# Kernel tuning notes

Measured on AMD Instinct MI355X. Metric: run time of the kernel, lower is better.

## Reference

```python
import jax, jax.numpy as jnp
import numpy as np

B, S, R, A, DW, DR = 64, 32, 128, 64, 512, 512

def setup_inputs() -> dict:
    key = jax.random.key(0)
    ks = jax.random.split(key, 12)
    s = 0.02
    return {
        "b_question_vector": jax.random.normal(ks[0], (B, S, DW), jnp.float32),
        "b_question_mask": jnp.zeros((B, S), dtype=bool),  # True = padding
        "b_r_space": jax.random.randint(ks[1], (B, A), 0, R),
        "b_coverage_t": jax.random.uniform(ks[2], (B, S), jnp.float32),
        "rel_emb": jax.random.normal(ks[3], (R, DR), jnp.float32) * s,
        "Wq": jax.random.normal(ks[4], (DR, DW), jnp.float32) * s,
        "bq": jnp.zeros((DR,), jnp.float32),
        "Wr": jax.random.normal(ks[5], (DR, DR), jnp.float32) * s,
        "br": jnp.zeros((DR,), jnp.float32),
        "Wc": jax.random.normal(ks[6], (DR, 1), jnp.float32) * s,
        "bc": jnp.zeros((DR,), jnp.float32),
        "Watt": jax.random.normal(ks[7], (1, DR), jnp.float32) * s,
        "batt": jnp.zeros((1,), jnp.float32),
    }

def reference(b_question_vector, b_question_mask, b_r_space, b_coverage_t,
              rel_emb, Wq, bq, Wr, br, Wc, bc, Watt, batt):
    # question_linear: [B,S,DW] -> [B,S,DR] (computed once, not repeated R times)
    qp = jnp.einsum('bsw,dw->bsd', b_question_vector, Wq) + bq
    # relation_linear over full embedding table: [R,DR]
    rp = rel_emb @ Wr.T + br
    # coverage_linear: Linear(1, DR) applied to scalar coverage -> [B,S,DR]
    cp = b_coverage_t[:, :, None] * Wc[:, 0] + bc
    # additive attention features, broadcast instead of repeat+view: [B,R,S,DR]
    feat = jnp.tanh(qp[:, None, :, :] + rp[None, :, None, :] + cp[:, None, :, :])
    # W_att: [B,R,S,DR] -> [B,R,S]
    scores = jnp.einsum('brsd,d->brs', feat, Watt[0]) + batt[0]
    scores = jnp.where(b_question_mask[:, None, :], -jnp.inf, scores)
    alpha = jax.nn.softmax(scores, axis=-1)                      # softmax over seq
    ctx = jnp.einsum('brs,bsw->brw', alpha, b_question_vector)   # [B,R,DW]
    # per-batch gather output_i[relation_i] (vectorized)
    out = jnp.take_along_axis(ctx, b_r_space[:, :, None], axis=1)    # [B,A,DW]
    alpha_sel = jnp.take_along_axis(alpha, b_r_space[:, :, None], axis=1)  # [B,A,S]
    return (out, alpha_sel)
```

## Files before the change

### kernel.cpp

```cpp
#include <hip/hip_runtime.h>
#include <hip/hip_bf16.h>
#include <math.h>

#define B_  64
#define S_  32
#define R_  128
#define A_  64
#define DW_ 512
#define DR_ 512

typedef __attribute__((ext_vector_type(8))) short short8;
typedef __attribute__((ext_vector_type(4))) float f32x4;

__device__ __forceinline__ unsigned short bf16_rn(float x) {
    union { float f; unsigned u; } v; v.f = x;
    unsigned r = v.u + 0x7FFF + ((v.u >> 16) & 1);
    return (unsigned short)(r >> 16);
}
__device__ __forceinline__ float bf16_to_f(unsigned short h) {
    union { unsigned u; float f; } v; v.u = ((unsigned)h) << 16;
    return v.f;
}

__device__ __forceinline__ int swz(int row, int chunk) {
    return row * 32 + ((chunk ^ ((row >> 1) & 3)) << 3);
}

__global__ __launch_bounds__(256) void gemm_dual_kernel(
    const float* __restrict__ A0, const float* __restrict__ B0, float* __restrict__ C0,
    int M0, int N0, int K0,
    const float* __restrict__ bias1_0, const float* __restrict__ bias2_0,
    const float* __restrict__ rowv0, const float* __restrict__ colv0,
    const float* __restrict__ A1, const float* __restrict__ B1, float* __restrict__ C1,
    int M1, int N1, int K1,
    const float* __restrict__ bias1_1)
{
    const int z = blockIdx.z;
    const float* Am; const float* Bm; float* C;
    const float *bias1, *bias2, *rowv, *colv;
    int M, N, K;
    if (z == 0) {
        Am = A0; Bm = B0; C = C0; M = M0; N = N0; K = K0;
        bias1 = bias1_0; bias2 = bias2_0; rowv = rowv0; colv = colv0;
    } else {
        Am = A1; Bm = B1; C = C1; M = M1; N = N1; K = K1;
        bias1 = bias1_1; bias2 = nullptr; rowv = nullptr; colv = nullptr;
    }

    const int bm = blockIdx.x * 64;
    const int bn = blockIdx.y * 64;
    if (bm >= M || bn >= N) return;

    __shared__ unsigned short Ahi[64 * 32], Alo[64 * 32];
    __shared__ unsigned short Bhi[64 * 32], Blo[64 * 32];

    const int tid  = threadIdx.x;
    const int l    = tid & 63;
    const int w    = tid >> 6;
    const int wr   = w >> 1;
    const int wc   = w & 1;
    const int fr   = l & 15;
    const int fc   = l >> 4;
    const int srow = tid >> 2;
    const int sch  = tid & 3;

    f32x4 acc[2][2] = {};

    float4 ra0, ra1, rb0, rb1;
    {
        const size_t arow = (size_t)(bm + srow) * K + sch * 8;
        const size_t brow = (size_t)(bn + srow) * K + sch * 8;
        ra0 = *(const float4*)&Am[arow];     ra1 = *(const float4*)&Am[arow + 4];
        rb0 = *(const float4*)&Bm[brow];     rb1 = *(const float4*)&Bm[brow + 4];
    }

    const int nsteps = K >> 5;
    for (int s = 0; s < nsteps; ++s) {
        short8 ahi, alo, bhi, blo;
        {
            float af[8] = {ra0.x, ra0.y, ra0.z, ra0.w, ra1.x, ra1.y, ra1.z, ra1.w};
            float bf[8] = {rb0.x, rb0.y, rb0.z, rb0.w, rb1.x, rb1.y, rb1.z, rb1.w};
            #pragma unroll
            for (int e = 0; e < 8; ++e) {
                unsigned short h = bf16_rn(af[e]);
                ahi[e] = (short)h;
                alo[e] = (short)bf16_rn(af[e] - bf16_to_f(h));
                unsigned short g = bf16_rn(bf[e]);
                bhi[e] = (short)g;
                blo[e] = (short)bf16_rn(bf[e] - bf16_to_f(g));
            }
        }
        __syncthreads();
        *(short8*)&Ahi[swz(srow, sch)] = ahi;
        *(short8*)&Alo[swz(srow, sch)] = alo;
        *(short8*)&Bhi[swz(srow, sch)] = bhi;
        *(short8*)&Blo[swz(srow, sch)] = blo;
        __syncthreads();

        if (s + 1 < nsteps) {
            const int k0 = (s + 1) << 5;
            const size_t arow = (size_t)(bm + srow) * K + k0 + sch * 8;
            const size_t brow = (size_t)(bn + srow) * K + k0 + sch * 8;
            ra0 = *(const float4*)&Am[arow];     ra1 = *(const float4*)&Am[arow + 4];
            rb0 = *(const float4*)&Bm[brow];     rb1 = *(const float4*)&Bm[brow + 4];
        }

        short8 fahi[2], falo[2], fbhi[2], fblo[2];
        #pragma unroll
        for (int i = 0; i < 2; ++i) {
            const int r = wr * 32 + i * 16 + fr;
            fahi[i] = *(const short8*)&Ahi[swz(r, fc)];
            falo[i] = *(const short8*)&Alo[swz(r, fc)];
            const int c = wc * 32 + i * 16 + fr;
            fbhi[i] = *(const short8*)&Bhi[swz(c, fc)];
            fblo[i] = *(const short8*)&Blo[swz(c, fc)];
        }
        #pragma unroll
        for (int i = 0; i < 2; ++i)
            #pragma unroll
            for (int j = 0; j < 2; ++j) {
                acc[i][j] = __builtin_amdgcn_mfma_f32_16x16x32_bf16(fahi[i], fbhi[j], acc[i][j], 0, 0, 0);
                acc[i][j] = __builtin_amdgcn_mfma_f32_16x16x32_bf16(fahi[i], fblo[j], acc[i][j], 0, 0, 0);
                acc[i][j] = __builtin_amdgcn_mfma_f32_16x16x32_bf16(falo[i], fbhi[j], acc[i][j], 0, 0, 0);
            }
    }

    #pragma unroll
    for (int i = 0; i < 2; ++i)
        #pragma unroll
        for (int j = 0; j < 2; ++j) {
            const int n  = bn + wc * 32 + j * 16 + fr;
            const float b1 = bias1[n];
            const float b2 = bias2 ? bias2[n] : 0.0f;
            const float cv = colv ? colv[n] : 0.0f;
            #pragma unroll
            for (int reg = 0; reg < 4; ++reg) {
                const int m = bm + wr * 32 + i * 16 + fc * 4 + reg;
                float v = acc[i][j][reg] + b1 + b2;
                if (rowv) v += rowv[m] * cv;
                C[(size_t)m * N + n] = v;
            }
        }
}

__global__ __launch_bounds__(256) void attn_kernel(
    const float* __restrict__ u,
    const float* __restrict__ rp,
    const float* __restrict__ watt,
    const float* __restrict__ battp,
    const float* __restrict__ qv,
    const unsigned char* __restrict__ mask,
    const int* __restrict__ rspace,
    float* __restrict__ out,
    float* __restrict__ alpha_out)
{
    const int blk  = blockIdx.x;
    const int b    = blk >> 4;
    const int ba0  = b * A_ + ((blk & 15) << 2);
    const int tid  = threadIdx.x;
    const int lane = tid & 63;
    const int wave = tid >> 6;

    const float K2 = 2.8853900817779268f;

    __shared__ float s_scores[4][S_];
    __shared__ float s_alpha[4][S_];

    float wav[8], rp2[4][8];
    {
        const float4* wa4 = (const float4*)watt;
        #pragma unroll
        for (int v = 0; v < 2; ++v) {
            float4 w = wa4[v * 64 + lane];
            wav[v*4+0] = w.x; wav[v*4+1] = w.y; wav[v*4+2] = w.z; wav[v*4+3] = w.w;
        }
        #pragma unroll
        for (int g = 0; g < 4; ++g) {
            const float4* rp4 = (const float4*)(rp + (size_t)rspace[ba0 + g] * DR_);
            #pragma unroll
            for (int v = 0; v < 2; ++v) {
                float4 t = rp4[v * 64 + lane];
                rp2[g][v*4+0] = t.x * K2; rp2[g][v*4+1] = t.y * K2;
                rp2[g][v*4+2] = t.z * K2; rp2[g][v*4+3] = t.w * K2;
            }
        }
    }
    const float batt = battp[0];

    float swa = wav[0] + wav[1] + wav[2] + wav[3] + wav[4] + wav[5] + wav[6] + wav[7];
    #pragma unroll
    for (int off = 32; off > 0; off >>= 1)
        swa += __shfl_xor(swa, off);

    #pragma unroll
    for (int si = 0; si < 8; ++si) {
        const int s = (wave << 3) + si;
        const float4* u4 = (const float4*)(u + ((size_t)b * S_ + s) * DR_);
        float uu[8];
        #pragma unroll
        for (int v = 0; v < 2; ++v) {
            float4 t = u4[v * 64 + lane];
            uu[v*4+0] = t.x; uu[v*4+1] = t.y; uu[v*4+2] = t.z; uu[v*4+3] = t.w;
        }
        float ac0 = 0.0f, ac1 = 0.0f, ac2 = 0.0f, ac3 = 0.0f;
        #pragma unroll
        for (int e = 0; e < 8; ++e) {
            const float ue = uu[e];
            const float we = wav[e];
            float z0 = __builtin_amdgcn_exp2f(fmaf(ue, K2, rp2[0][e]));
            float z1 = __builtin_amdgcn_exp2f(fmaf(ue, K2, rp2[1][e]));
            float z2 = __builtin_amdgcn_exp2f(fmaf(ue, K2, rp2[2][e]));
            float z3 = __builtin_amdgcn_exp2f(fmaf(ue, K2, rp2[3][e]));
            ac0 = fmaf(we, __builtin_amdgcn_rcpf(z0 + 1.0f), ac0);
            ac1 = fmaf(we, __builtin_amdgcn_rcpf(z1 + 1.0f), ac1);
            ac2 = fmaf(we, __builtin_amdgcn_rcpf(z2 + 1.0f), ac2);
            ac3 = fmaf(we, __builtin_amdgcn_rcpf(z3 + 1.0f), ac3);
        }
        #pragma unroll
        for (int off = 32; off > 0; off >>= 1) {
            ac0 += __shfl_xor(ac0, off);
            ac1 += __shfl_xor(ac1, off);
            ac2 += __shfl_xor(ac2, off);
            ac3 += __shfl_xor(ac3, off);
        }
        if (lane == 0) {
            s_scores[0][s] = fmaf(-2.0f, ac0, swa) + batt;
            s_scores[1][s] = fmaf(-2.0f, ac1, swa) + batt;
            s_scores[2][s] = fmaf(-2.0f, ac2, swa) + batt;
            s_scores[3][s] = fmaf(-2.0f, ac3, swa) + batt;
        }
    }
    __syncthreads();

    if (tid < 128) {
        const int g = tid >> 5;
        const int s = tid & 31;
        float sc = s_scores[g][s];
        if (mask[b * S_ + s]) sc = -INFINITY;
        float m = sc;
        #pragma unroll
        for (int off = 16; off > 0; off >>= 1)
            m = fmaxf(m, __shfl_xor(m, off));
        float e = __expf(sc - m);
        float sum = e;
        #pragma unroll
        for (int off = 16; off > 0; off >>= 1)
            sum += __shfl_xor(sum, off);
        float al = e / sum;
        s_alpha[g][s] = al;
        alpha_out[(size_t)(ba0 + g) * S_ + s] = al;
    }
    __syncthreads();

    float2 acc[4] = {};
    const float* qb = qv + (size_t)b * S_ * DW_;
    #pragma unroll 4
    for (int s = 0; s < S_; ++s) {
        float2 q = *(const float2*)&qb[s * DW_ + tid * 2];
        #pragma unroll
        for (int g = 0; g < 4; ++g) {
            const float al = s_alpha[g][s];
            acc[g].x = fmaf(al, q.x, acc[g].x);
            acc[g].y = fmaf(al, q.y, acc[g].y);
        }
    }
    #pragma unroll
    for (int g = 0; g < 4; ++g)
        *(float2*)&out[(size_t)(ba0 + g) * DW_ + tid * 2] = acc[g];
}

extern "C" void kernel_launch(void* const* d_in, const int* in_sizes, int n_in,
                              void* d_out, int out_size, void* d_ws, size_t ws_size,
                              hipStream_t stream) {
    const float*         qv   = (const float*)d_in[0];
    const unsigned char* mask = (const unsigned char*)d_in[1];
    const int*           rsp  = (const int*)d_in[2];
    const float*         cov  = (const float*)d_in[3];
    const float*         rel  = (const float*)d_in[4];
    const float*         Wq   = (const float*)d_in[5];
    const float*         bq   = (const float*)d_in[6];
    const float*         Wr   = (const float*)d_in[7];
    const float*         br   = (const float*)d_in[8];
    const float*         Wc   = (const float*)d_in[9];
    const float*         bc   = (const float*)d_in[10];
    const float*         Watt = (const float*)d_in[11];
    const float*         batt = (const float*)d_in[12];

    float* u  = (float*)d_ws;
    float* rp = u + (size_t)B_ * S_ * DR_;

    float* out       = (float*)d_out;
    float* alpha_out = out + (size_t)B_ * A_ * DW_;

    dim3 blk(256);

    gemm_dual_kernel<<<dim3((B_ * S_) / 64, DR_ / 64, 2), blk, 0, stream>>>(
        qv, Wq, u, B_ * S_, DR_, DW_, bq, bc, cov, Wc,
        rel, Wr, rp, R_, DR_, DR_, br);

    attn_kernel<<<dim3(B_ * (A_ / 4)), blk, 0, stream>>>(
        u, rp, Watt, batt, qv, mask, rsp, out, alpha_out);
}
```

Measured before the change: 120.2 us.

## Double-buffer GEMM shared tiles and process eight relations per attention block

The GEMM kernel now double-buffers its LDS tiles. The next tile's bf16 hi/lo split and store happen after the MFMAs, so each k-step needs one barrier instead of two. The attention kernel handles 8 selected relations per block instead of 4. This halves the grid and amortizes the u-row loads and the question-vector pass over twice as many relations. The cost is twice the LDS in the GEMM, more registers in the attention kernel (rp2[8][8], 8 accumulators), and fewer blocks to hide latency.

```diff
diff --git a/kernel.cpp b/kernel.cpp
--- a/kernel.cpp
+++ b/kernel.cpp
@@ -51,8 +51,8 @@
     const int bn = blockIdx.y * 64;
     if (bm >= M || bn >= N) return;
 
-    __shared__ unsigned short Ahi[64 * 32], Alo[64 * 32];
-    __shared__ unsigned short Bhi[64 * 32], Blo[64 * 32];
+    __shared__ unsigned short Ahi[2][64 * 32], Alo[2][64 * 32];
+    __shared__ unsigned short Bhi[2][64 * 32], Blo[2][64 * 32];
 
     const int tid  = threadIdx.x;
     const int l    = tid & 63;
@@ -67,17 +67,64 @@
     f32x4 acc[2][2] = {};
 
     float4 ra0, ra1, rb0, rb1;
+
     {
         const size_t arow = (size_t)(bm + srow) * K + sch * 8;
         const size_t brow = (size_t)(bn + srow) * K + sch * 8;
         ra0 = *(const float4*)&Am[arow];     ra1 = *(const float4*)&Am[arow + 4];
         rb0 = *(const float4*)&Bm[brow];     rb1 = *(const float4*)&Bm[brow + 4];
-    }
+
+        short8 ahi, alo, bhi, blo;
+        float af[8] = {ra0.x, ra0.y, ra0.z, ra0.w, ra1.x, ra1.y, ra1.z, ra1.w};
+        float bf[8] = {rb0.x, rb0.y, rb0.z, rb0.w, rb1.x, rb1.y, rb1.z, rb1.w};
+        #pragma unroll
+        for (int e = 0; e < 8; ++e) {
+            unsigned short h = bf16_rn(af[e]);
+            ahi[e] = (short)h;
+            alo[e] = (short)bf16_rn(af[e] - bf16_to_f(h));
+            unsigned short g = bf16_rn(bf[e]);
+            bhi[e] = (short)g;
+            blo[e] = (short)bf16_rn(bf[e] - bf16_to_f(g));
+        }
+        *(short8*)&Ahi[0][swz(srow, sch)] = ahi;
+        *(short8*)&Alo[0][swz(srow, sch)] = alo;
+        *(short8*)&Bhi[0][swz(srow, sch)] = bhi;
+        *(short8*)&Blo[0][swz(srow, sch)] = blo;
+    }
+    __syncthreads();
 
     const int nsteps = K >> 5;
+    int cur = 0;
     for (int s = 0; s < nsteps; ++s) {
-        short8 ahi, alo, bhi, blo;
-        {
+        if (s + 1 < nsteps) {
+            const int k0 = (s + 1) << 5;
+            const size_t arow = (size_t)(bm + srow) * K + k0 + sch * 8;
+            const size_t brow = (size_t)(bn + srow) * K + k0 + sch * 8;
+            ra0 = *(const float4*)&Am[arow];     ra1 = *(const float4*)&Am[arow + 4];
+            rb0 = *(const float4*)&Bm[brow];     rb1 = *(const float4*)&Bm[brow + 4];
+        }
+
+        short8 fahi[2], falo[2], fbhi[2], fblo[2];
+        #pragma unroll
+        for (int i = 0; i < 2; ++i) {
+            const int r = wr * 32 + i * 16 + fr;
+            fahi[i] = *(const short8*)&Ahi[cur][swz(r, fc)];
+            falo[i] = *(const short8*)&Alo[cur][swz(r, fc)];
+            const int c = wc * 32 + i * 16 + fr;
+            fbhi[i] = *(const short8*)&Bhi[cur][swz(c, fc)];
+            fblo[i] = *(const short8*)&Blo[cur][swz(c, fc)];
+        }
+        #pragma unroll
+        for (int i = 0; i < 2; ++i)
+            #pragma unroll
+            for (int j = 0; j < 2; ++j) {
+                acc[i][j] = __builtin_amdgcn_mfma_f32_16x16x32_bf16(fahi[i], fbhi[j], acc[i][j], 0, 0, 0);
+                acc[i][j] = __builtin_amdgcn_mfma_f32_16x16x32_bf16(fahi[i], fblo[j], acc[i][j], 0, 0, 0);
+                acc[i][j] = __builtin_amdgcn_mfma_f32_16x16x32_bf16(falo[i], fbhi[j], acc[i][j], 0, 0, 0);
+            }
+
+        if (s + 1 < nsteps) {
+            short8 ahi, alo, bhi, blo;
             float af[8] = {ra0.x, ra0.y, ra0.z, ra0.w, ra1.x, ra1.y, ra1.z, ra1.w};
             float bf[8] = {rb0.x, rb0.y, rb0.z, rb0.w, rb1.x, rb1.y, rb1.z, rb1.w};
             #pragma unroll
@@ -89,40 +136,14 @@
                 bhi[e] = (short)g;
                 blo[e] = (short)bf16_rn(bf[e] - bf16_to_f(g));
             }
-        }
-        __syncthreads();
-        *(short8*)&Ahi[swz(srow, sch)] = ahi;
-        *(short8*)&Alo[swz(srow, sch)] = alo;
-        *(short8*)&Bhi[swz(srow, sch)] = bhi;
-        *(short8*)&Blo[swz(srow, sch)] = blo;
-        __syncthreads();
-
-        if (s + 1 < nsteps) {
-            const int k0 = (s + 1) << 5;
-            const size_t arow = (size_t)(bm + srow) * K + k0 + sch * 8;
-            const size_t brow = (size_t)(bn + srow) * K + k0 + sch * 8;
-            ra0 = *(const float4*)&Am[arow];     ra1 = *(const float4*)&Am[arow + 4];
-            rb0 = *(const float4*)&Bm[brow];     rb1 = *(const float4*)&Bm[brow + 4];
-        }
-
-        short8 fahi[2], falo[2], fbhi[2], fblo[2];
-        #pragma unroll
-        for (int i = 0; i < 2; ++i) {
-            const int r = wr * 32 + i * 16 + fr;
-            fahi[i] = *(const short8*)&Ahi[swz(r, fc)];
-            falo[i] = *(const short8*)&Alo[swz(r, fc)];
-            const int c = wc * 32 + i * 16 + fr;
-            fbhi[i] = *(const short8*)&Bhi[swz(c, fc)];
-            fblo[i] = *(const short8*)&Blo[swz(c, fc)];
-        }
-        #pragma unroll
-        for (int i = 0; i < 2; ++i)
-            #pragma unroll
-            for (int j = 0; j < 2; ++j) {
-                acc[i][j] = __builtin_amdgcn_mfma_f32_16x16x32_bf16(fahi[i], fbhi[j], acc[i][j], 0, 0, 0);
-                acc[i][j] = __builtin_amdgcn_mfma_f32_16x16x32_bf16(fahi[i], fblo[j], acc[i][j], 0, 0, 0);
-                acc[i][j] = __builtin_amdgcn_mfma_f32_16x16x32_bf16(falo[i], fbhi[j], acc[i][j], 0, 0, 0);
-            }
+            const int nxt = cur ^ 1;
+            *(short8*)&Ahi[nxt][swz(srow, sch)] = ahi;
+            *(short8*)&Alo[nxt][swz(srow, sch)] = alo;
+            *(short8*)&Bhi[nxt][swz(srow, sch)] = bhi;
+            *(short8*)&Blo[nxt][swz(srow, sch)] = blo;
+            __syncthreads();
+            cur = nxt;
+        }
     }
 
     #pragma unroll
@@ -155,18 +176,18 @@
     float* __restrict__ alpha_out)
 {
     const int blk  = blockIdx.x;
-    const int b    = blk >> 4;
-    const int ba0  = b * A_ + ((blk & 15) << 2);
+    const int b    = blk >> 3;
+    const int ba0  = b * A_ + ((blk & 7) << 3);
     const int tid  = threadIdx.x;
     const int lane = tid & 63;
     const int wave = tid >> 6;
 
     const float K2 = 2.8853900817779268f;
 
-    __shared__ float s_scores[4][S_];
-    __shared__ float s_alpha[4][S_];
-
-    float wav[8], rp2[4][8];
+    __shared__ float s_scores[8][S_];
+    __shared__ float s_alpha[8][S_];
+
+    float wav[8], rp2[8][8];
     {
         const float4* wa4 = (const float4*)watt;
         #pragma unroll
@@ -175,7 +196,7 @@
             wav[v*4+0] = w.x; wav[v*4+1] = w.y; wav[v*4+2] = w.z; wav[v*4+3] = w.w;
         }
         #pragma unroll
-        for (int g = 0; g < 4; ++g) {
+        for (int g = 0; g < 8; ++g) {
             const float4* rp4 = (const float4*)(rp + (size_t)rspace[ba0 + g] * DR_);
             #pragma unroll
             for (int v = 0; v < 2; ++v) {
@@ -202,37 +223,31 @@
             float4 t = u4[v * 64 + lane];
             uu[v*4+0] = t.x; uu[v*4+1] = t.y; uu[v*4+2] = t.z; uu[v*4+3] = t.w;
         }
-        float ac0 = 0.0f, ac1 = 0.0f, ac2 = 0.0f, ac3 = 0.0f;
+        float ac[8] = {};
         #pragma unroll
         for (int e = 0; e < 8; ++e) {
             const float ue = uu[e];
             const float we = wav[e];
-            float z0 = __builtin_amdgcn_exp2f(fmaf(ue, K2, rp2[0][e]));
-            float z1 = __builtin_amdgcn_exp2f(fmaf(ue, K2, rp2[1][e]));
-            float z2 = __builtin_amdgcn_exp2f(fmaf(ue, K2, rp2[2][e]));
-            float z3 = __builtin_amdgcn_exp2f(fmaf(ue, K2, rp2[3][e]));
-            ac0 = fmaf(we, __builtin_amdgcn_rcpf(z0 + 1.0f), ac0);
-            ac1 = fmaf(we, __builtin_amdgcn_rcpf(z1 + 1.0f), ac1);
-            ac2 = fmaf(we, __builtin_amdgcn_rcpf(z2 + 1.0f), ac2);
-            ac3 = fmaf(we, __builtin_amdgcn_rcpf(z3 + 1.0f), ac3);
-        }
-        #pragma unroll
-        for (int off = 32; off > 0; off >>= 1) {
-            ac0 += __shfl_xor(ac0, off);
-            ac1 += __shfl_xor(ac1, off);
-            ac2 += __shfl_xor(ac2, off);
-            ac3 += __shfl_xor(ac3, off);
-        }
-        if (lane == 0) {
-            s_scores[0][s] = fmaf(-2.0f, ac0, swa) + batt;
-            s_scores[1][s] = fmaf(-2.0f, ac1, swa) + batt;
-            s_scores[2][s] = fmaf(-2.0f, ac2, swa) + batt;
-            s_scores[3][s] = fmaf(-2.0f, ac3, swa) + batt;
-        }
+            const float uk = ue * K2;
+            #pragma unroll
+            for (int g = 0; g < 8; ++g) {
+                float zz = __builtin_amdgcn_exp2f(uk + rp2[g][e]);
+                ac[g] = fmaf(we, __builtin_amdgcn_rcpf(zz + 1.0f), ac[g]);
+            }
+        }
+        #pragma unroll
+        for (int off = 32; off > 0; off >>= 1)
+            #pragma unroll
+            for (int g = 0; g < 8; ++g)
+                ac[g] += __shfl_xor(ac[g], off);
+        if (lane == 0)
+            #pragma unroll
+            for (int g = 0; g < 8; ++g)
+                s_scores[g][s] = fmaf(-2.0f, ac[g], swa) + batt;
     }
     __syncthreads();
 
-    if (tid < 128) {
+    {
         const int g = tid >> 5;
         const int s = tid & 31;
         float sc = s_scores[g][s];
@@ -252,21 +267,21 @@
     }
     __syncthreads();
 
-    float2 acc[4] = {};
+    float2 acc2[8] = {};
     const float* qb = qv + (size_t)b * S_ * DW_;
     #pragma unroll 4
     for (int s = 0; s < S_; ++s) {
         float2 q = *(const float2*)&qb[s * DW_ + tid * 2];
         #pragma unroll
-        for (int g = 0; g < 4; ++g) {
+        for (int g = 0; g < 8; ++g) {
             const float al = s_alpha[g][s];
-            acc[g].x = fmaf(al, q.x, acc[g].x);
-            acc[g].y = fmaf(al, q.y, acc[g].y);
+            acc2[g].x = fmaf(al, q.x, acc2[g].x);
+            acc2[g].y = fmaf(al, q.y, acc2[g].y);
         }
     }
     #pragma unroll
-    for (int g = 0; g < 4; ++g)
-        *(float2*)&out[(size_t)(ba0 + g) * DW_ + tid * 2] = acc[g];
+    for (int g = 0; g < 8; ++g)
+        *(float2*)&out[(size_t)(ba0 + g) * DW_ + tid * 2] = acc2[g];
 }
 
 extern "C" void kernel_launch(void* const* d_in, const int* in_sizes, int n_in,
@@ -298,6 +313,6 @@
         qv, Wq, u, B_ * S_, DR_, DW_, bq, bc, cov, Wc,
         rel, Wr, rp, R_, DR_, DR_, br);
 
-    attn_kernel<<<dim3(B_ * (A_ / 4)), blk, 0, stream>>>(
+    attn_kernel<<<dim3(B_ * (A_ / 8)), blk, 0, stream>>>(
         u, rp, Watt, batt, qv, mask, rsp, out, alpha_out);
 }
```

Measured after the change: 120.7 us. Within noise of the previous version (+0.4%).
